# Optimization experiments

Hardware: AMD Instinct MI355X
Metric: run time of the kernel (lower is better)

The kernel has to match this reference:

```python
import jax, jax.numpy as jnp
import numpy as np

N = 100000   # nodes
E = 3200000  # edges (avg degree 32)
G = 64       # graphs in batch
IN_DIM, HID, NCLS = 260, 128, 16


def setup_inputs() -> dict:
    key = jax.random.key(0)
    ks = jax.random.split(key, 14)

    def lin_w(k, fan_in, fan_out):
        return (jax.random.normal(k, (fan_in, fan_out), jnp.float32)
                / np.float32(np.sqrt(fan_in)))

    return {
        "x": jax.random.normal(ks[0], (N, IN_DIM), jnp.float32),
        "edge_index": jax.random.randint(ks[1], (2, E), 0, N, dtype=jnp.int32),
        "batch": jnp.sort(jax.random.randint(ks[2], (N,), 0, G, dtype=jnp.int32)),
        "w1": lin_w(ks[3], IN_DIM, HID), "b1": jnp.zeros((HID,), jnp.float32),
        "w2": lin_w(ks[4], HID, HID),    "b2": jnp.zeros((HID,), jnp.float32),
        "w3": lin_w(ks[5], HID, HID),    "b3": jnp.zeros((HID,), jnp.float32),
        "fc1_w": lin_w(ks[6], HID, 128), "fc1_b": jnp.zeros((128,), jnp.float32),
        "fc2_w": lin_w(ks[7], 128, NCLS),"fc2_b": jnp.zeros((NCLS,), jnp.float32),
    }


def reference(x, edge_index, batch, w1, b1, w2, b2, w3, b3,
              fc1_w, fc1_b, fc2_w, fc2_b):
    # --- GCN normalization (PyG GCNConv default: add self-loops, D^-1/2 A D^-1/2)
    loops = jnp.arange(N, dtype=edge_index.dtype)
    src = jnp.concatenate([edge_index[0], loops])  # [E+N]
    dst = jnp.concatenate([edge_index[1], loops])  # [E+N]
    deg = jax.ops.segment_sum(jnp.ones_like(dst, jnp.float32), dst,
                              num_segments=N)      # in-degree incl. self-loop
    dinv = jnp.where(deg > 0, jax.lax.rsqrt(deg), 0.0)
    norm = (dinv[src] * dinv[dst])[:, None]        # [E+N, 1]

    def gcn_conv(h, w, b):
        h = h @ w                                  # dense transform first
        msg = h[src] * norm                        # gather + scale  [E+N, HID]
        out = jax.ops.segment_sum(msg, dst, num_segments=N)  # scatter-add
        return out + b

    h = jax.nn.relu(gcn_conv(x, w1, b1))
    h = jax.nn.relu(gcn_conv(h, w2, b2))
    h = jax.nn.relu(gcn_conv(h, w3, b3))

    # --- global mean pool over graph ids
    sums = jax.ops.segment_sum(h, batch, num_segments=G)                # [G, HID]
    cnts = jax.ops.segment_sum(jnp.ones((N,), jnp.float32), batch, G)   # [G]
    pooled = sums / jnp.maximum(cnts, 1.0)[:, None]

    # --- MLP head
    z = jax.nn.relu(pooled @ fc1_w + fc1_b)
    return z @ fc2_w + fc2_b                       # [G, NCLS]
```

## Files before the change

kernel.cpp:

```cpp
#include <hip/hip_runtime.h>

#define HID 128
#define SCAN_CHUNK 1024

#define NB 256
#define BW 400
#define DEPTH 24
#define CH 2048

typedef __attribute__((ext_vector_type(8))) short bf16x8;
typedef __attribute__((ext_vector_type(4))) float f32x4;

__device__ inline float blo(unsigned u) { return __uint_as_float(u << 16); }
__device__ inline float bhi(unsigned u) { return __uint_as_float(u & 0xffff0000u); }
__device__ inline unsigned rne16(float x) {
  unsigned u = __float_as_uint(x);
  return (u + 0x7fffu + ((u >> 16) & 1u)) >> 16;
}
__device__ inline unsigned pk2(float a, float b) { return (rne16(b) << 16) | rne16(a); }

__global__ void k_init(float* __restrict__ psum, int* __restrict__ gstart,
                       int* __restrict__ bhist, int G) {
  int i = blockIdx.x * 256 + threadIdx.x;
  if (i < G * HID) psum[i] = 0.f;
  if (i <= G) gstart[i] = -1;
  if (i < NB) bhist[i] = 0;
}

__device__ inline void prep_one(const float* __restrict__ W, unsigned* __restrict__ Wt,
                                int K, int KP2, int b) {
  int idx = b * 256 + threadIdx.x;
  if (idx >= 128 * KP2) return;
  int c = idx / KP2, kk = idx - c * KP2;
  int k0 = kk * 2, k1 = k0 + 1;
  float v0 = (k0 < K) ? W[(long)k0 * 128 + c] : 0.f;
  float v1 = (k1 < K) ? W[(long)k1 * 128 + c] : 0.f;
  Wt[idx] = pk2(v0, v1);
}

__global__ void k_prep_w3(const float* __restrict__ w1, const float* __restrict__ w2,
                          const float* __restrict__ w3, unsigned* __restrict__ Wt1,
                          unsigned* __restrict__ Wt2, unsigned* __restrict__ Wt3,
                          int IN) {
  int b = blockIdx.x;
  if (b < 72) prep_one(w1, Wt1, IN, 144, b);
  else if (b < 104) prep_one(w2, Wt2, 128, 64, b - 72);
  else prep_one(w3, Wt3, 128, 64, b - 104);
}

__global__ __launch_bounds__(256) void k_hist(const int* __restrict__ dst, int E, int N,
                                              int* __restrict__ bhist) {
  __shared__ int h[NB];
  int t = threadIdx.x;
  h[t] = 0;
  __syncthreads();
  int i = blockIdx.x * blockDim.x + t;
  int stride = gridDim.x * blockDim.x;
  for (; i < E; i += stride) {
    int b = (int)(((long long)dst[i] * NB) / N);
    atomicAdd(&h[b], 1);
  }
  __syncthreads();
  if (h[t]) atomicAdd(&bhist[t], h[t]);
}

__global__ __launch_bounds__(NB) void k_bscan(const int* __restrict__ bhist,
                                              int* __restrict__ bstart,
                                              int* __restrict__ gcur, int E) {
  __shared__ int sh[NB];
  int t = threadIdx.x;
  int v = bhist[t];
  sh[t] = v;
  __syncthreads();
  for (int off = 1; off < NB; off <<= 1) {
    int x = (t >= off) ? sh[t - off] : 0;
    __syncthreads();
    sh[t] += x;
    __syncthreads();
  }
  int excl = sh[t] - v;
  bstart[t] = excl;
  gcur[t] = excl;
  if (t == NB - 1) bstart[NB] = sh[t];
}

__global__ __launch_bounds__(256) void k_scatter(const int* __restrict__ src,
                                                 const int* __restrict__ dst,
                                                 int E, int N,
                                                 unsigned long long* __restrict__ binned,
                                                 int* __restrict__ gcur) {
  __shared__ unsigned long long buf[NB][DEPTH];
  __shared__ int cnt[NB];
  int t = threadIdx.x;
  long cover = (long)gridDim.x * CH;
  int nround = (int)((E + cover - 1) / cover);
  for (int r = 0; r < nround; ++r) {
    cnt[t] = 0;
    __syncthreads();
    long base = (long)r * cover + (long)blockIdx.x * CH;
#pragma unroll
    for (int k = 0; k < CH / 256; ++k) {
      long i = base + k * 256 + t;
      if (i < E) {
        int s = src[i], d = dst[i];
        int b = (int)(((long long)d * NB) / N);
        unsigned long long pack =
            ((unsigned long long)(unsigned)d << 32) | (unsigned)s;
        int slot = atomicAdd(&cnt[b], 1);
        if (slot < DEPTH) buf[b][slot] = pack;
        else { int g = atomicAdd(&gcur[b], 1); binned[g] = pack; }
      }
    }
    __syncthreads();
    {
      int c = cnt[t];
      if (c > DEPTH) c = DEPTH;
      if (c > 0) {
        int g = atomicAdd(&gcur[t], c);
        for (int k = 0; k < c; ++k) binned[g + k] = buf[t][k];
      }
    }
    __syncthreads();
  }
}

__global__ __launch_bounds__(256) void k_bdeg(const unsigned long long* __restrict__ binned,
                                              const int* __restrict__ bstart, int N,
                                              int* __restrict__ deg,
                                              float* __restrict__ dinv) {
  __shared__ int hist[BW];
  int b = blockIdx.x;
  int t = threadIdx.x;
  int d0 = (int)(((long long)b * N + NB - 1) / NB);
  int d1 = (int)(((long long)(b + 1) * N + NB - 1) / NB);
  if (d1 > N) d1 = N;
  int W = d1 - d0;
  for (int w = t; w < W; w += 256) hist[w] = 0;
  __syncthreads();
  int s = bstart[b], e = bstart[b + 1];
  for (int i = s + t; i < e; i += 256) {
    int d = (int)(binned[i] >> 32);
    atomicAdd(&hist[d - d0], 1);
  }
  __syncthreads();
  for (int w = t; w < W; w += 256) {
    int dv = hist[w];
    deg[d0 + w] = dv;
    dinv[d0 + w] = rsqrtf((float)(dv + 1));
  }
}

__global__ void k_scan_block_sums(const int* __restrict__ deg, int N, int* __restrict__ bsum) {
  __shared__ int sh[256];
  int base = blockIdx.x * SCAN_CHUNK;
  int t = threadIdx.x;
  int s = 0;
#pragma unroll
  for (int j = 0; j < 4; ++j) {
    int idx = base + t * 4 + j;
    if (idx < N) s += deg[idx];
  }
  sh[t] = s;
  __syncthreads();
  for (int off = 128; off > 0; off >>= 1) {
    if (t < off) sh[t] += sh[t + off];
    __syncthreads();
  }
  if (t == 0) bsum[blockIdx.x] = sh[0];
}

__global__ __launch_bounds__(256) void k_scan_offsets(const int* __restrict__ bsum, int nb,
                                                      int* __restrict__ boff) {
  __shared__ int sh[256];
  int t = threadIdx.x;
  int v = (t < nb) ? bsum[t] : 0;
  sh[t] = v;
  __syncthreads();
  for (int off = 1; off < 256; off <<= 1) {
    int x = (t >= off) ? sh[t - off] : 0;
    __syncthreads();
    sh[t] += x;
    __syncthreads();
  }
  if (t < nb) boff[t] = sh[t] - v;
}

__global__ void k_scan_write(const int* __restrict__ deg, int N,
                             const int* __restrict__ boff, int* __restrict__ rowstart) {
  __shared__ int sh[256];
  int base = blockIdx.x * SCAN_CHUNK;
  int t = threadIdx.x;
  int v[4];
  int s = 0;
#pragma unroll
  for (int j = 0; j < 4; ++j) {
    int idx = base + t * 4 + j;
    v[j] = (idx < N) ? deg[idx] : 0;
    s += v[j];
  }
  sh[t] = s;
  __syncthreads();
  for (int off = 1; off < 256; off <<= 1) {
    int x = 0;
    if (t >= off) x = sh[t - off];
    __syncthreads();
    sh[t] += x;
    __syncthreads();
  }
  int excl = sh[t] - s;
  int run = boff[blockIdx.x] + excl;
#pragma unroll
  for (int j = 0; j < 4; ++j) {
    int idx = base + t * 4 + j;
    if (idx < N) rowstart[idx] = run;
    run += v[j];
  }
}

__global__ __launch_bounds__(256) void k_place(const unsigned long long* __restrict__ binned,
                                               const int* __restrict__ bstart,
                                               const int* __restrict__ rowstart, int N,
                                               int* __restrict__ csr) {
  __shared__ int cur[BW];
  int b = blockIdx.x;
  int t = threadIdx.x;
  int d0 = (int)(((long long)b * N + NB - 1) / NB);
  int d1 = (int)(((long long)(b + 1) * N + NB - 1) / NB);
  if (d1 > N) d1 = N;
  int W = d1 - d0;
  for (int w = t; w < W; w += 256) cur[w] = 0;
  __syncthreads();
  int s = bstart[b], e = bstart[b + 1];
  for (int i = s + t; i < e; i += 256) {
    unsigned long long p = binned[i];
    int d = (int)(p >> 32);
    int sn = (int)(p & 0xffffffffu);
    int pos = rowstart[d] + atomicAdd(&cur[d - d0], 1);
    csr[pos] = sn;
  }
}

__global__ __launch_bounds__(256) void k_gemm_mf(const unsigned* __restrict__ A,
                                                 const unsigned* __restrict__ Wt,
                                                 const float* __restrict__ dscale,
                                                 unsigned* __restrict__ Cu, int N) {
  int t = threadIdx.x;
  int w = t >> 6;
  int l = t & 63;
  int lr = l & 15;
  int kg = l >> 4;
  int wr0 = blockIdx.x * 128 + w * 32;

  f32x4 acc[2][8];
#pragma unroll
  for (int rt = 0; rt < 2; ++rt)
#pragma unroll
    for (int f = 0; f < 8; ++f) acc[rt][f] = (f32x4){0.f, 0.f, 0.f, 0.f};

  int r0 = wr0 + lr, r1 = wr0 + 16 + lr;
#pragma unroll
  for (int kt = 0; kt < 4; ++kt) {
    int ko = kt * 16 + kg * 4;
    bf16x8 a0 = {}, a1 = {};
    if (r0 < N) a0 = *(const bf16x8*)&A[(long)r0 * 64 + ko];
    if (r1 < N) a1 = *(const bf16x8*)&A[(long)r1 * 64 + ko];
#pragma unroll
    for (int f = 0; f < 8; ++f) {
      bf16x8 b = *(const bf16x8*)&Wt[(f * 16 + lr) * 64 + ko];
      acc[0][f] = __builtin_amdgcn_mfma_f32_16x16x32_bf16(a0, b, acc[0][f], 0, 0, 0);
      acc[1][f] = __builtin_amdgcn_mfma_f32_16x16x32_bf16(a1, b, acc[1][f], 0, 0, 0);
    }
  }
#pragma unroll
  for (int rt = 0; rt < 2; ++rt) {
#pragma unroll
    for (int reg = 0; reg < 4; ++reg) {
      int row = wr0 + rt * 16 + kg * 4 + reg;
      float ds = (row < N) ? dscale[row] : 0.f;
#pragma unroll
      for (int f = 0; f < 8; ++f) {
        float v = acc[rt][f][reg] * ds;
        float pv = __shfl_xor(v, 1);
        if (!(l & 1) && row < N)
          Cu[(long)row * 64 + ((f * 16 + lr) >> 1)] = pk2(v, pv);
      }
    }
  }
}

__global__ __launch_bounds__(256) void k_gemm1_mf(const float* __restrict__ X,
                                                  const unsigned* __restrict__ Wt,
                                                  const float* __restrict__ dscale,
                                                  unsigned* __restrict__ Cu, int N, int K) {
  int t = threadIdx.x;
  int w = t >> 6;
  int l = t & 63;
  int lr = l & 15;
  int kg = l >> 4;
  int wr0 = blockIdx.x * 128 + w * 32;

  f32x4 acc[2][8];
#pragma unroll
  for (int rt = 0; rt < 2; ++rt)
#pragma unroll
    for (int f = 0; f < 8; ++f) acc[rt][f] = (f32x4){0.f, 0.f, 0.f, 0.f};

  int r0 = wr0 + lr, r1 = wr0 + 16 + lr;
  int nkt = (K + 31) / 32;
  for (int kt = 0; kt < nkt; ++kt) {
    int kb = kt * 32 + kg * 8;
    bf16x8 a0 = {}, a1 = {};
    if (kb + 7 < K) {
      if (r0 < N) {
        const float* p = &X[(long)r0 * K + kb];
        float4 u = *(const float4*)p, v = *(const float4*)(p + 4);
        union { uint4 q; bf16x8 b; } cv;
        cv.q.x = pk2(u.x, u.y); cv.q.y = pk2(u.z, u.w);
        cv.q.z = pk2(v.x, v.y); cv.q.w = pk2(v.z, v.w);
        a0 = cv.b;
      }
      if (r1 < N) {
        const float* p = &X[(long)r1 * K + kb];
        float4 u = *(const float4*)p, v = *(const float4*)(p + 4);
        union { uint4 q; bf16x8 b; } cv;
        cv.q.x = pk2(u.x, u.y); cv.q.y = pk2(u.z, u.w);
        cv.q.z = pk2(v.x, v.y); cv.q.w = pk2(v.z, v.w);
        a1 = cv.b;
      }
    } else if (kb < K) {
      float t0[8], t1[8];
#pragma unroll
      for (int j = 0; j < 8; ++j) {
        int k = kb + j;
        t0[j] = (r0 < N && k < K) ? X[(long)r0 * K + k] : 0.f;
        t1[j] = (r1 < N && k < K) ? X[(long)r1 * K + k] : 0.f;
      }
      union { uint4 q; bf16x8 b; } c0, c1;
      c0.q.x = pk2(t0[0], t0[1]); c0.q.y = pk2(t0[2], t0[3]);
      c0.q.z = pk2(t0[4], t0[5]); c0.q.w = pk2(t0[6], t0[7]);
      c1.q.x = pk2(t1[0], t1[1]); c1.q.y = pk2(t1[2], t1[3]);
      c1.q.z = pk2(t1[4], t1[5]); c1.q.w = pk2(t1[6], t1[7]);
      a0 = c0.b; a1 = c1.b;
    }
    int ko = kt * 16 + kg * 4;
#pragma unroll
    for (int f = 0; f < 8; ++f) {
      bf16x8 b = *(const bf16x8*)&Wt[(f * 16 + lr) * 144 + ko];
      acc[0][f] = __builtin_amdgcn_mfma_f32_16x16x32_bf16(a0, b, acc[0][f], 0, 0, 0);
      acc[1][f] = __builtin_amdgcn_mfma_f32_16x16x32_bf16(a1, b, acc[1][f], 0, 0, 0);
    }
  }
#pragma unroll
  for (int rt = 0; rt < 2; ++rt) {
#pragma unroll
    for (int reg = 0; reg < 4; ++reg) {
      int row = wr0 + rt * 16 + kg * 4 + reg;
      float ds = (row < N) ? dscale[row] : 0.f;
#pragma unroll
      for (int f = 0; f < 8; ++f) {
        float v = acc[rt][f][reg] * ds;
        float pv = __shfl_xor(v, 1);
        if (!(l & 1) && row < N)
          Cu[(long)row * 64 + ((f * 16 + lr) >> 1)] = pk2(v, pv);
      }
    }
  }
}

__global__ __launch_bounds__(256) void k_agg(const uint4* __restrict__ T4,
                                             const float* __restrict__ dinv,
                                             const int* __restrict__ rowstart,
                                             const int* __restrict__ deg,
                                             const int* __restrict__ csr,
                                             const float* __restrict__ bias,
                                             uint4* __restrict__ outu,
                                             int N) {
  int t = threadIdx.x;
  int grp = t >> 4;
  int lane = t & 15;
  int i = blockIdx.x * 16 + grp;
  if (i >= N) return;

  int c0 = lane * 8;
  float b0 = bias[c0 + 0], b1 = bias[c0 + 1], b2 = bias[c0 + 2], b3 = bias[c0 + 3];
  float b4 = bias[c0 + 4], b5 = bias[c0 + 5], b6 = bias[c0 + 6], b7 = bias[c0 + 7];

  uint4 su = T4[(long)i * 16 + lane];
  float a0 = blo(su.x), a1 = bhi(su.x), a2 = blo(su.y), a3 = bhi(su.y);
  float a4 = blo(su.z), a5 = bhi(su.z), a6 = blo(su.w), a7 = bhi(su.w);

  int s0 = rowstart[i];
  int d = deg[i];
  int j = 0;
  for (; j + 3 < d; j += 4) {
    int n1 = csr[s0 + j];
    int n2 = csr[s0 + j + 1];
    int n3 = csr[s0 + j + 2];
    int n4 = csr[s0 + j + 3];
    uint4 u1 = T4[(long)n1 * 16 + lane];
    uint4 u2 = T4[(long)n2 * 16 + lane];
    uint4 u3 = T4[(long)n3 * 16 + lane];
    uint4 u4 = T4[(long)n4 * 16 + lane];
    a0 += (blo(u1.x) + blo(u2.x)) + (blo(u3.x) + blo(u4.x));
    a1 += (bhi(u1.x) + bhi(u2.x)) + (bhi(u3.x) + bhi(u4.x));
    a2 += (blo(u1.y) + blo(u2.y)) + (blo(u3.y) + blo(u4.y));
    a3 += (bhi(u1.y) + bhi(u2.y)) + (bhi(u3.y) + bhi(u4.y));
    a4 += (blo(u1.z) + blo(u2.z)) + (blo(u3.z) + blo(u4.z));
    a5 += (bhi(u1.z) + bhi(u2.z)) + (bhi(u3.z) + bhi(u4.z));
    a6 += (blo(u1.w) + blo(u2.w)) + (blo(u3.w) + blo(u4.w));
    a7 += (bhi(u1.w) + bhi(u2.w)) + (bhi(u3.w) + bhi(u4.w));
  }
  for (; j < d; ++j) {
    int n1 = csr[s0 + j];
    uint4 u1 = T4[(long)n1 * 16 + lane];
    a0 += blo(u1.x); a1 += bhi(u1.x); a2 += blo(u1.y); a3 += bhi(u1.y);
    a4 += blo(u1.z); a5 += bhi(u1.z); a6 += blo(u1.w); a7 += bhi(u1.w);
  }
  float di = dinv[i];
  float v0 = fmaxf(di * a0 + b0, 0.f);
  float v1 = fmaxf(di * a1 + b1, 0.f);
  float v2 = fmaxf(di * a2 + b2, 0.f);
  float v3 = fmaxf(di * a3 + b3, 0.f);
  float v4 = fmaxf(di * a4 + b4, 0.f);
  float v5 = fmaxf(di * a5 + b5, 0.f);
  float v6 = fmaxf(di * a6 + b6, 0.f);
  float v7 = fmaxf(di * a7 + b7, 0.f);
  uint4 o;
  o.x = pk2(v0, v1); o.y = pk2(v2, v3); o.z = pk2(v4, v5); o.w = pk2(v6, v7);
  outu[(long)i * 16 + lane] = o;
}

__global__ void k_starts(const int* __restrict__ batch, int N, int* __restrict__ start) {
  int i = blockIdx.x * blockDim.x + threadIdx.x;
  int stride = gridDim.x * blockDim.x;
  for (; i < N; i += stride) {
    int g = batch[i];
    if (i == 0) {
      start[g] = 0;
    } else if (batch[i - 1] != g) {
      start[g] = i;
    }
  }
}

__global__ __launch_bounds__(256) void k_fix_starts(int* __restrict__ start, int G, int N) {
  __shared__ int sh[256];
  int t = threadIdx.x;
  int v = (t < G) ? start[t] : N;
  if (v < 0) v = N;
  sh[t] = v;
  __syncthreads();
  for (int off = 1; off < 256; off <<= 1) {
    int x = (t + off < 256) ? sh[t + off] : N;
    int nv = min(sh[t], x);
    __syncthreads();
    sh[t] = nv;
    __syncthreads();
  }
  if (t < G) start[t] = sh[t];
  if (t == 0) start[G] = N;
}

__global__ __launch_bounds__(256) void k_pool2(const unsigned* __restrict__ hu,
                                               const int* __restrict__ batch,
                                               float* __restrict__ psum, int N) {
  int t = threadIdx.x;
  int rg = t >> 6;
  int lane = t & 63;
  long base = (long)blockIdx.x * 64;
  float a0 = 0.f, a1 = 0.f;
  int cur = -1;
#pragma unroll
  for (int j = 0; j < 16; ++j) {
    long r = base + j * 4 + rg;
    if (r >= N) break;
    int g = batch[r];
    if (g != cur) {
      if (cur >= 0) {
        atomicAdd(&psum[cur * HID + lane * 2], a0);
        atomicAdd(&psum[cur * HID + lane * 2 + 1], a1);
        a0 = 0.f; a1 = 0.f;
      }
      cur = g;
    }
    unsigned u = hu[r * 64 + lane];
    a0 += blo(u); a1 += bhi(u);
  }
  if (cur >= 0) {
    atomicAdd(&psum[cur * HID + lane * 2], a0);
    atomicAdd(&psum[cur * HID + lane * 2 + 1], a1);
  }
}

__global__ __launch_bounds__(128) void k_head(const float* __restrict__ psum,
                                              const int* __restrict__ gstart,
                                              const float* __restrict__ fc1w,
                                              const float* __restrict__ fc1b,
                                              const float* __restrict__ fc2w,
                                              const float* __restrict__ fc2b,
                                              float* __restrict__ out, int G) {
  __shared__ float pooled[HID];
  __shared__ float z1[HID];
  int g = blockIdx.x;
  int c = threadIdx.x;
  float cn = fmaxf((float)(gstart[g + 1] - gstart[g]), 1.f);
  pooled[c] = psum[g * HID + c] / cn;
  __syncthreads();
  float a = fc1b[c];
#pragma unroll 8
  for (int k = 0; k < HID; ++k) a += pooled[k] * fc1w[k * HID + c];
  z1[c] = fmaxf(a, 0.f);
  __syncthreads();
  if (c < 16) {
    float o = fc2b[c];
#pragma unroll 8
    for (int k = 0; k < HID; ++k) o += z1[k] * fc2w[k * 16 + c];
    out[g * 16 + c] = o;
  }
}

extern "C" void kernel_launch(void* const* d_in, const int* in_sizes, int n_in,
                              void* d_out, int out_size, void* d_ws, size_t ws_size,
                              hipStream_t stream) {
  const float* x     = (const float*)d_in[0];
  const int*   ei    = (const int*)d_in[1];
  const int*   batch = (const int*)d_in[2];
  const float* w1    = (const float*)d_in[3];
  const float* b1    = (const float*)d_in[4];
  const float* w2    = (const float*)d_in[5];
  const float* b2    = (const float*)d_in[6];
  const float* w3    = (const float*)d_in[7];
  const float* b3    = (const float*)d_in[8];
  const float* fc1w  = (const float*)d_in[9];
  const float* fc1b  = (const float*)d_in[10];
  const float* fc2w  = (const float*)d_in[11];
  const float* fc2b  = (const float*)d_in[12];
  float* out = (float*)d_out;

  const int IN = in_sizes[3] / HID;
  const int N  = in_sizes[0] / IN;
  const int E  = in_sizes[1] / 2;
  const int G  = out_size / 16;

  const int* srcp = ei;
  const int* dstp = ei + E;

  char* wsp = (char*)d_ws;
  auto alloc = [&](size_t bytes) {
    char* p = wsp;
    wsp += (bytes + 255) & ~(size_t)255;
    return p;
  };
  int*   deg      = (int*)alloc((size_t)N * 4);
  int*   rowstart = (int*)alloc((size_t)N * 4);
  int*   bsum     = (int*)alloc(1024 * 4);
  int*   boff     = (int*)alloc(1024 * 4);
  int*   bhist    = (int*)alloc(NB * 4);
  int*   bstart   = (int*)alloc((NB + 1) * 4);
  int*   gcur     = (int*)alloc(NB * 4);
  int*   gstart   = (int*)alloc((size_t)(G + 1) * 4);
  float* dinv     = (float*)alloc((size_t)N * 4);
  float* psum     = (float*)alloc((size_t)G * HID * 4);
  unsigned* Wt1   = (unsigned*)alloc(128 * 144 * 4);
  unsigned* Wt2   = (unsigned*)alloc(128 * 64 * 4);
  unsigned* Wt3   = (unsigned*)alloc(128 * 64 * 4);
  int*   csr      = (int*)alloc((size_t)E * 4);
  unsigned* bufA  = (unsigned*)alloc((size_t)N * 64 * 4);
  unsigned* bufB  = (unsigned*)alloc((size_t)N * 64 * 4);
  unsigned long long* binned = (unsigned long long*)bufA;

  k_init<<<32, 256, 0, stream>>>(psum, gstart, bhist, G);
  k_prep_w3<<<136, 256, 0, stream>>>(w1, w2, w3, Wt1, Wt2, Wt3, IN);

  k_hist<<<512, 256, 0, stream>>>(dstp, E, N, bhist);
  k_bscan<<<1, NB, 0, stream>>>(bhist, bstart, gcur, E);
  k_scatter<<<782, 256, 0, stream>>>(srcp, dstp, E, N, binned, gcur);
  k_bdeg<<<NB, 256, 0, stream>>>(binned, bstart, N, deg, dinv);

  int nb = (N + SCAN_CHUNK - 1) / SCAN_CHUNK;
  k_scan_block_sums<<<nb, 256, 0, stream>>>(deg, N, bsum);
  k_scan_offsets<<<1, 256, 0, stream>>>(bsum, nb, boff);
  k_scan_write<<<nb, 256, 0, stream>>>(deg, N, boff, rowstart);
  k_place<<<NB, 256, 0, stream>>>(binned, bstart, rowstart, N, csr);

  k_starts<<<256, 256, 0, stream>>>(batch, N, gstart);
  k_fix_starts<<<1, 256, 0, stream>>>(gstart, G, N);

  int gblocks = (N + 127) / 128;
  int ablocks = (N + 15) / 16;
  k_gemm1_mf<<<gblocks, 256, 0, stream>>>(x, Wt1, dinv, bufA, N, IN);
  k_agg<<<ablocks, 256, 0, stream>>>((const uint4*)bufA, dinv, rowstart, deg, csr, b1,
                                     (uint4*)bufB, N);

  k_gemm_mf<<<gblocks, 256, 0, stream>>>(bufB, Wt2, dinv, bufA, N);
  k_agg<<<ablocks, 256, 0, stream>>>((const uint4*)bufA, dinv, rowstart, deg, csr, b2,
                                     (uint4*)bufB, N);

  k_gemm_mf<<<gblocks, 256, 0, stream>>>(bufB, Wt3, dinv, bufA, N);
  k_agg<<<ablocks, 256, 0, stream>>>((const uint4*)bufA, dinv, rowstart, deg, csr, b3,
                                     (uint4*)bufB, N);

  int pblocks = (N + 63) / 64;
  k_pool2<<<pblocks, 256, 0, stream>>>(bufB, batch, psum, N);
  k_head<<<G, 128, 0, stream>>>(psum, gstart, fc1w, fc1b, fc2w, fc2b, out, G);
}
```

Measured before the change: 609.5 us.

## Fuse CSR build into one per-bucket kernel with packed 32-bit edge keys

Replaces the separate degree, three-pass global scan and placement kernels with a single per-bucket kernel that histograms local degrees, scans them in shared memory and places edges, using the bucket start as the global row offset. Edge records shrink from 64-bit (dst,src) to 32-bit (local dst<<17 | src), halving binned traffic. The init kernel is merged into the weight prep kernel. This removes several launches and global round trips. The 17-bit source field limits N to 131072 and local offsets to below 32768.

Result: faster. 580.3 us (-4.8%).

```diff
diff --git a/kernel.cpp b/kernel.cpp
--- a/kernel.cpp
+++ b/kernel.cpp
@@ -1,7 +1,6 @@
 #include <hip/hip_runtime.h>
 
 #define HID 128
-#define SCAN_CHUNK 1024
 
 #define NB 256
 #define BW 400
@@ -18,14 +17,6 @@
   return (u + 0x7fffu + ((u >> 16) & 1u)) >> 16;
 }
 __device__ inline unsigned pk2(float a, float b) { return (rne16(b) << 16) | rne16(a); }
-
-__global__ void k_init(float* __restrict__ psum, int* __restrict__ gstart,
-                       int* __restrict__ bhist, int G) {
-  int i = blockIdx.x * 256 + threadIdx.x;
-  if (i < G * HID) psum[i] = 0.f;
-  if (i <= G) gstart[i] = -1;
-  if (i < NB) bhist[i] = 0;
-}
 
 __device__ inline void prep_one(const float* __restrict__ W, unsigned* __restrict__ Wt,
                                 int K, int KP2, int b) {
@@ -38,14 +29,21 @@
   Wt[idx] = pk2(v0, v1);
 }
 
-__global__ void k_prep_w3(const float* __restrict__ w1, const float* __restrict__ w2,
-                          const float* __restrict__ w3, unsigned* __restrict__ Wt1,
-                          unsigned* __restrict__ Wt2, unsigned* __restrict__ Wt3,
-                          int IN) {
+__global__ void k_prep_init(const float* __restrict__ w1, const float* __restrict__ w2,
+                            const float* __restrict__ w3, unsigned* __restrict__ Wt1,
+                            unsigned* __restrict__ Wt2, unsigned* __restrict__ Wt3,
+                            float* __restrict__ psum, int* __restrict__ gstart,
+                            int* __restrict__ bhist, int IN, int G) {
   int b = blockIdx.x;
   if (b < 72) prep_one(w1, Wt1, IN, 144, b);
   else if (b < 104) prep_one(w2, Wt2, 128, 64, b - 72);
   else prep_one(w3, Wt3, 128, 64, b - 104);
+  if (b < 32) {
+    int i = b * 256 + threadIdx.x;
+    if (i < G * HID) psum[i] = 0.f;
+    if (i <= G) gstart[i] = -1;
+    if (i < NB) bhist[i] = 0;
+  }
 }
 
 __global__ __launch_bounds__(256) void k_hist(const int* __restrict__ dst, int E, int N,
@@ -87,9 +85,9 @@
 __global__ __launch_bounds__(256) void k_scatter(const int* __restrict__ src,
                                                  const int* __restrict__ dst,
                                                  int E, int N,
-                                                 unsigned long long* __restrict__ binned,
+                                                 unsigned* __restrict__ binned,
                                                  int* __restrict__ gcur) {
-  __shared__ unsigned long long buf[NB][DEPTH];
+  __shared__ unsigned buf[NB][DEPTH];
   __shared__ int cnt[NB];
   int t = threadIdx.x;
   long cover = (long)gridDim.x * CH;
@@ -104,8 +102,8 @@
       if (i < E) {
         int s = src[i], d = dst[i];
         int b = (int)(((long long)d * NB) / N);
-        unsigned long long pack =
-            ((unsigned long long)(unsigned)d << 32) | (unsigned)s;
+        int d0 = (int)(((long long)b * N + NB - 1) / NB);
+        unsigned pack = ((unsigned)(d - d0) << 17) | (unsigned)s;
         int slot = atomicAdd(&cnt[b], 1);
         if (slot < DEPTH) buf[b][slot] = pack;
         else { int g = atomicAdd(&gcur[b], 1); binned[g] = pack; }
@@ -124,118 +122,59 @@
   }
 }
 
-__global__ __launch_bounds__(256) void k_bdeg(const unsigned long long* __restrict__ binned,
-                                              const int* __restrict__ bstart, int N,
-                                              int* __restrict__ deg,
-                                              float* __restrict__ dinv) {
+__global__ __launch_bounds__(256) void k_build(const unsigned* __restrict__ binned,
+                                               const int* __restrict__ bstart, int N,
+                                               int* __restrict__ deg,
+                                               float* __restrict__ dinv,
+                                               int* __restrict__ rowstart,
+                                               int* __restrict__ csr) {
   __shared__ int hist[BW];
+  __shared__ int loc[BW];
+  __shared__ int scanbuf[256];
   int b = blockIdx.x;
   int t = threadIdx.x;
   int d0 = (int)(((long long)b * N + NB - 1) / NB);
   int d1 = (int)(((long long)(b + 1) * N + NB - 1) / NB);
   if (d1 > N) d1 = N;
   int W = d1 - d0;
-  for (int w = t; w < W; w += 256) hist[w] = 0;
+  for (int w = t; w < BW; w += 256) hist[w] = 0;
   __syncthreads();
   int s = bstart[b], e = bstart[b + 1];
+  for (int i = s + t; i < e; i += 256)
+    atomicAdd(&hist[binned[i] >> 17], 1);
+  __syncthreads();
+  int e0 = t * 2, e1 = t * 2 + 1;
+  int h0 = (e0 < W) ? hist[e0] : 0;
+  int h1 = (e1 < W) ? hist[e1] : 0;
+  scanbuf[t] = h0 + h1;
+  __syncthreads();
+  for (int off = 1; off < 256; off <<= 1) {
+    int x = (t >= off) ? scanbuf[t - off] : 0;
+    __syncthreads();
+    scanbuf[t] += x;
+    __syncthreads();
+  }
+  int excl = scanbuf[t] - (h0 + h1);
+  if (e0 < W) loc[e0] = excl;
+  if (e1 < W) loc[e1] = excl + h0;
+  if (e0 < W) {
+    deg[d0 + e0] = h0;
+    dinv[d0 + e0] = rsqrtf((float)(h0 + 1));
+    rowstart[d0 + e0] = s + loc[e0];
+    hist[e0] = 0;
+  }
+  if (e1 < W) {
+    deg[d0 + e1] = h1;
+    dinv[d0 + e1] = rsqrtf((float)(h1 + 1));
+    rowstart[d0 + e1] = s + loc[e1];
+    hist[e1] = 0;
+  }
+  __syncthreads();
   for (int i = s + t; i < e; i += 256) {
-    int d = (int)(binned[i] >> 32);
-    atomicAdd(&hist[d - d0], 1);
-  }
-  __syncthreads();
-  for (int w = t; w < W; w += 256) {
-    int dv = hist[w];
-    deg[d0 + w] = dv;
-    dinv[d0 + w] = rsqrtf((float)(dv + 1));
-  }
-}
-
-__global__ void k_scan_block_sums(const int* __restrict__ deg, int N, int* __restrict__ bsum) {
-  __shared__ int sh[256];
-  int base = blockIdx.x * SCAN_CHUNK;
-  int t = threadIdx.x;
-  int s = 0;
-#pragma unroll
-  for (int j = 0; j < 4; ++j) {
-    int idx = base + t * 4 + j;
-    if (idx < N) s += deg[idx];
-  }
-  sh[t] = s;
-  __syncthreads();
-  for (int off = 128; off > 0; off >>= 1) {
-    if (t < off) sh[t] += sh[t + off];
-    __syncthreads();
-  }
-  if (t == 0) bsum[blockIdx.x] = sh[0];
-}
-
-__global__ __launch_bounds__(256) void k_scan_offsets(const int* __restrict__ bsum, int nb,
-                                                      int* __restrict__ boff) {
-  __shared__ int sh[256];
-  int t = threadIdx.x;
-  int v = (t < nb) ? bsum[t] : 0;
-  sh[t] = v;
-  __syncthreads();
-  for (int off = 1; off < 256; off <<= 1) {
-    int x = (t >= off) ? sh[t - off] : 0;
-    __syncthreads();
-    sh[t] += x;
-    __syncthreads();
-  }
-  if (t < nb) boff[t] = sh[t] - v;
-}
-
-__global__ void k_scan_write(const int* __restrict__ deg, int N,
-                             const int* __restrict__ boff, int* __restrict__ rowstart) {
-  __shared__ int sh[256];
-  int base = blockIdx.x * SCAN_CHUNK;
-  int t = threadIdx.x;
-  int v[4];
-  int s = 0;
-#pragma unroll
-  for (int j = 0; j < 4; ++j) {
-    int idx = base + t * 4 + j;
-    v[j] = (idx < N) ? deg[idx] : 0;
-    s += v[j];
-  }
-  sh[t] = s;
-  __syncthreads();
-  for (int off = 1; off < 256; off <<= 1) {
-    int x = 0;
-    if (t >= off) x = sh[t - off];
-    __syncthreads();
-    sh[t] += x;
-    __syncthreads();
-  }
-  int excl = sh[t] - s;
-  int run = boff[blockIdx.x] + excl;
-#pragma unroll
-  for (int j = 0; j < 4; ++j) {
-    int idx = base + t * 4 + j;
-    if (idx < N) rowstart[idx] = run;
-    run += v[j];
-  }
-}
-
-__global__ __launch_bounds__(256) void k_place(const unsigned long long* __restrict__ binned,
-                                               const int* __restrict__ bstart,
-                                               const int* __restrict__ rowstart, int N,
-                                               int* __restrict__ csr) {
-  __shared__ int cur[BW];
-  int b = blockIdx.x;
-  int t = threadIdx.x;
-  int d0 = (int)(((long long)b * N + NB - 1) / NB);
-  int d1 = (int)(((long long)(b + 1) * N + NB - 1) / NB);
-  if (d1 > N) d1 = N;
-  int W = d1 - d0;
-  for (int w = t; w < W; w += 256) cur[w] = 0;
-  __syncthreads();
-  int s = bstart[b], e = bstart[b + 1];
-  for (int i = s + t; i < e; i += 256) {
-    unsigned long long p = binned[i];
-    int d = (int)(p >> 32);
-    int sn = (int)(p & 0xffffffffu);
-    int pos = rowstart[d] + atomicAdd(&cur[d - d0], 1);
+    unsigned p = binned[i];
+    int dl = (int)(p >> 17);
+    int sn = (int)(p & 0x1ffffu);
+    int pos = s + loc[dl] + atomicAdd(&hist[dl], 1);
     csr[pos] = sn;
   }
 }
@@ -553,8 +492,6 @@
   };
   int*   deg      = (int*)alloc((size_t)N * 4);
   int*   rowstart = (int*)alloc((size_t)N * 4);
-  int*   bsum     = (int*)alloc(1024 * 4);
-  int*   boff     = (int*)alloc(1024 * 4);
   int*   bhist    = (int*)alloc(NB * 4);
   int*   bstart   = (int*)alloc((NB + 1) * 4);
   int*   gcur     = (int*)alloc(NB * 4);
@@ -567,21 +504,15 @@
   int*   csr      = (int*)alloc((size_t)E * 4);
   unsigned* bufA  = (unsigned*)alloc((size_t)N * 64 * 4);
   unsigned* bufB  = (unsigned*)alloc((size_t)N * 64 * 4);
-  unsigned long long* binned = (unsigned long long*)bufA;
-
-  k_init<<<32, 256, 0, stream>>>(psum, gstart, bhist, G);
-  k_prep_w3<<<136, 256, 0, stream>>>(w1, w2, w3, Wt1, Wt2, Wt3, IN);
+  unsigned* binned = (unsigned*)bufA;
+
+  k_prep_init<<<136, 256, 0, stream>>>(w1, w2, w3, Wt1, Wt2, Wt3,
+                                       psum, gstart, bhist, IN, G);
 
   k_hist<<<512, 256, 0, stream>>>(dstp, E, N, bhist);
   k_bscan<<<1, NB, 0, stream>>>(bhist, bstart, gcur, E);
   k_scatter<<<782, 256, 0, stream>>>(srcp, dstp, E, N, binned, gcur);
-  k_bdeg<<<NB, 256, 0, stream>>>(binned, bstart, N, deg, dinv);
-
-  int nb = (N + SCAN_CHUNK - 1) / SCAN_CHUNK;
-  k_scan_block_sums<<<nb, 256, 0, stream>>>(deg, N, bsum);
-  k_scan_offsets<<<1, 256, 0, stream>>>(bsum, nb, boff);
-  k_scan_write<<<nb, 256, 0, stream>>>(deg, N, boff, rowstart);
-  k_place<<<NB, 256, 0, stream>>>(binned, bstart, rowstart, N, csr);
+  k_build<<<NB, 256, 0, stream>>>(binned, bstart, N, deg, dinv, rowstart, csr);
 
   k_starts<<<256, 256, 0, stream>>>(batch, N, gstart);
   k_fix_starts<<<1, 256, 0, stream>>>(gstart, G, N);
```
